# Kernel optimization log

Hardware: AMD Instinct MI355X
Metric: run time of the kernel (lower is better)

Reference implementation:

```python
import jax, jax.numpy as jnp
import numpy as np

B, T, F, U, L = 64, 700, 3, 400, 3


def setup_inputs() -> dict:
    key = jax.random.key(0)
    ks = jax.random.split(key, 10)
    s = 0.08  # small init to keep gates unsaturated
    return {
        "x": jax.random.normal(ks[0], (B, T, F), jnp.float32),
        "Wx0": jax.random.normal(ks[1], (F, 4 * U), jnp.float32) * s,
        "Wx1": jax.random.normal(ks[2], (U, 4 * U), jnp.float32) * s,
        "Wx2": jax.random.normal(ks[3], (U, 4 * U), jnp.float32) * s,
        "Wh": jax.random.normal(ks[4], (L, U, 4 * U), jnp.float32) * s,
        "b": jnp.zeros((L, 4 * U), jnp.float32),
        "pi": jax.random.normal(ks[5], (L, U), jnp.float32) * s,
        "pf": jax.random.normal(ks[6], (L, U), jnp.float32) * s,
        "po": jax.random.normal(ks[7], (L, U), jnp.float32) * s,
        "Wd": jax.random.normal(ks[8], (U, F), jnp.float32) * s,
        "bd": jnp.zeros((F,), jnp.float32),
    }


def _lstm_peephole_layer(x_tbd, Wx, Wh_l, b_l, pi_l, pf_l, po_l):
    """x_tbd: [T, B, D] -> [T, B, U] with peephole LSTM (Graves 2013)."""
    Bsz = x_tbd.shape[1]
    Uu = Wh_l.shape[0]
    # Precompute the input contribution for all timesteps in one GEMM.
    xp = jnp.einsum("tbd,dk->tbk", x_tbd, Wx) + b_l  # [T, B, 4U]

    def step(carry, zt):
        h, c = carry
        z = zt + h @ Wh_l  # [B, 4U]
        zi, zf, zg, zo = jnp.split(z, 4, axis=-1)
        i = jax.nn.sigmoid(zi + pi_l * c)
        f = jax.nn.sigmoid(zf + pf_l * c)
        c_new = f * c + i * jnp.tanh(zg)
        o = jax.nn.sigmoid(zo + po_l * c_new)
        h_new = o * jnp.tanh(c_new)
        return (h_new, c_new), h_new

    init = (jnp.zeros((Bsz, Uu), x_tbd.dtype), jnp.zeros((Bsz, Uu), x_tbd.dtype))
    _, hs = jax.lax.scan(step, init, xp)
    return hs  # [T, B, U]


def reference(x, Wx0, Wx1, Wx2, Wh, b, pi, pf, po, Wd, bd):
    h = jnp.transpose(x, (1, 0, 2))  # [T, B, F]
    for l, Wx in enumerate((Wx0, Wx1, Wx2)):
        h = _lstm_peephole_layer(h, Wx, Wh[l], b[l], pi[l], pf[l], po[l])
    out = jnp.einsum("tbu,uf->tbf", h, Wd) + bd
    return jnp.transpose(out, (1, 0, 2))  # [B, T, F]
```

## Files before the change

### kernel.cpp

```cpp
#include <hip/hip_runtime.h>
#include <hip/hip_fp16.h>
#include <math.h>

#define B_ 64
#define T_ 700
#define U_ 400
#define NF 704
#define FR_LS 13312

typedef _Float16 half8 __attribute__((ext_vector_type(8)));
typedef float float4v __attribute__((ext_vector_type(4)));

union AFrag { unsigned u[4]; half8 h; };

__device__ __forceinline__ unsigned agloadu(const unsigned* p) {
    return __hip_atomic_load(p, __ATOMIC_RELAXED, __HIP_MEMORY_SCOPE_AGENT);
}
__device__ __forceinline__ void agstoreu(unsigned* p, unsigned v) {
    __hip_atomic_store(p, v, __ATOMIC_RELAXED, __HIP_MEMORY_SCOPE_AGENT);
}
__device__ __forceinline__ float sig_(float v) {
    return __builtin_amdgcn_rcpf(1.f + __expf(-v));
}
__device__ __forceinline__ float tanh_(float v) {
    return 1.f - 2.f * __builtin_amdgcn_rcpf(__expf(2.f * v) + 1.f);
}
__device__ __forceinline__ void waitflag(const unsigned* f, unsigned target) {
    while (agloadu(f) < target) __builtin_amdgcn_s_sleep(2);
}
__device__ __forceinline__ unsigned f16u(float v) {
    union { _Float16 f; unsigned short s; } cv; cv.f = (_Float16)v; return (unsigned)cv.s;
}

__device__ __forceinline__ void pollfrag13(const unsigned* __restrict__ base,
                                           const unsigned par,
                                           AFrag* __restrict__ a, const int lane)
{
    {
        const unsigned* pp = base + (lane % 13) * 256 + ((lane * 37) & 255);
        while (!__all((int)(((agloadu(pp) ^ par) & 1u) == 0u)))
            __builtin_amdgcn_s_sleep(3);
    }
    unsigned pend = 0x1FFFu;
    do {
#pragma unroll
        for (int ck = 0; ck < 13; ++ck) if ((pend >> ck) & 1) {
#pragma unroll
            for (int d = 0; d < 4; ++d)
                a[ck].u[d] = agloadu(base + ck * 256 + d * 64 + lane);
        }
#pragma unroll
        for (int ck = 0; ck < 13; ++ck) if ((pend >> ck) & 1) {
            const unsigned m = (a[ck].u[0] ^ par) | (a[ck].u[1] ^ par)
                             | (a[ck].u[2] ^ par) | (a[ck].u[3] ^ par);
            if (__all((int)((m & 1u) == 0u))) pend &= ~(1u << ck);
        }
        if (pend) __builtin_amdgcn_s_sleep(3);
    } while (pend);
}

template<int DEPTH, int CP>
__global__ void __launch_bounds__(256, 1)
lstm_mix(const float* __restrict__ x,
         const float* __restrict__ Wx0,
         const float* __restrict__ Wx1,
         const float* __restrict__ Wx2,
         const float* __restrict__ Wh,
         const float* __restrict__ bias,
         const float* __restrict__ pi,
         const float* __restrict__ pf,
         const float* __restrict__ po,
         const float* __restrict__ Wd,
         const float* __restrict__ bd,
         float* __restrict__ out,
         unsigned* __restrict__ ws)
{
    __shared__ alignas(16) _Float16 wlds[26 * 512];
    __shared__ alignas(16) float zlds[4 * 528];
    __shared__ float gc[160];

    const int LW = NF * CP * 32;
    unsigned* F0 = ws;
    unsigned* F1 = F0 + LW;
    unsigned* F2 = F1 + LW;
    unsigned* FO = F2 + LW;
    unsigned* frag0 = ws + (size_t)4 * LW;

    const int blk  = blockIdx.x;
    const int tid  = threadIdx.x;
    const int lane = tid & 63;
    const int wv   = tid >> 6;
    const int cpi  = (blk + wv) & (CP - 1);

    int layer, u0;
    if      (blk < 50)  { layer = 0; u0 = blk * 8; }
    else if (blk < 150) { layer = 1; u0 = (blk - 50) * 4; }
    else if (blk < 250) { layer = 2; u0 = (blk - 150) * 4; }
    else                { layer = 3; u0 = 0; }

    const bool padw = (blk == 49) || (blk == 149) || (blk == 249);
    int pad_off[2];
    {
        const int i0 = tid, i1 = tid + 256;
        pad_off[0] = (i0 >> 7) * 3328 + 12 * 256 + (((i0 >> 4) & 3) * 64)
                   + (2 + ((i0 >> 6) & 1)) * 16 + (i0 & 15);
        pad_off[1] = (i1 >> 7) * 3328 + 12 * 256 + (((i1 >> 4) & 3) * 64)
                   + (2 + ((i1 >> 6) & 1)) * 16 + (i1 & 15);
    }

    {
        const float* __restrict__ Wxl = (layer == 1) ? Wx1 : Wx2;
        for (int i = tid; i < 26 * 64; i += 256) {
            const int ln = i & 63, ck = i >> 6;
            const int q = ln >> 4, nn = ln & 15;
            float vals[8];
#pragma unroll
            for (int j = 0; j < 8; ++j) {
                const int kc = ck % 13;
                const int k = kc * 32 + q * 8 + j;
                float v = 0.f;
                if (k < 400) {
                    if (layer == 0) {
                        const int col32 = (ck / 13) * 16 + nn;
                        const int gcol = (col32 >> 3) * U_ + u0 + (col32 & 7);
                        v = Wh[(size_t)k * 1600 + gcol];
                    } else if (layer < 3) {
                        const int gcol = (nn >> 2) * U_ + u0 + (nn & 3);
                        v = (ck >= 13) ? Wh[((size_t)layer * U_ + k) * 1600 + gcol]
                                       : Wxl[(size_t)k * 1600 + gcol];
                    } else {
                        if (ck < 13 && nn < 3) v = Wd[k * 3 + nn];
                    }
                }
                vals[j] = v;
            }
#pragma unroll
            for (int j = 0; j < 8; ++j)
                wlds[ck * 512 + ln * 8 + j] = (_Float16)vals[j];
        }
        if (layer == 0) {
            if (tid < 128) {
                const int col32 = tid >> 2, comp = tid & 3;
                const int gcol = (col32 >> 3) * U_ + u0 + (col32 & 7);
                gc[tid] = (comp == 0) ? bias[gcol] : Wx0[(size_t)(comp - 1) * 1600 + gcol];
            } else if (tid < 152) {
                const int idx = tid - 128, ul = idx / 3, j = idx - ul * 3;
                const float* pp = (j == 0) ? pi : (j == 1) ? pf : po;
                gc[tid] = pp[u0 + ul];
            }
        } else if (layer < 3) {
            if (tid < 16) {
                gc[tid] = bias[layer * 1600 + (tid >> 2) * U_ + u0 + (tid & 3)];
            } else if (tid < 28) {
                const int idx = tid - 16, ul = idx / 3, j = idx - ul * 3;
                const float* pp = (j == 0) ? pi : (j == 1) ? pf : po;
                gc[tid] = pp[layer * U_ + u0 + ul];
            }
        } else {
            if (tid < 3) gc[tid] = bd[tid];
        }
    }
    __syncthreads();

    const int wvz   = wv * 528;
    const int b_loc = lane & 15;
    const int quad  = lane >> 4;
    float cst[2] = {0.f, 0.f};

    for (int t = 0; t < T_; ++t) {
        const int sw = t % DEPTH;
        const int sr = (t + DEPTH - 1) % DEPTH;
        const unsigned pI = (unsigned)((t / DEPTH) & 1);
        const unsigned pO = (unsigned)(((t - 1) / DEPTH) & 1);

        float x0, x1, x2;
        if (layer == 0) {
            const size_t xb = (size_t)(wv * 16 + b_loc) * T_ + t;
            x0 = x[xb * 3 + 0]; x1 = x[xb * 3 + 1]; x2 = x[xb * 3 + 2];
        }

        if (lane == 0) {
            if (layer == 0) {
                if (wv == 0 && t >= DEPTH) waitflag(F1 + ((t - DEPTH) * CP + cpi) * 32, 100);
            } else if (layer == 1) {
                waitflag(F0 + (t * CP + cpi) * 32, 50);
                if (wv == 0 && t >= DEPTH) waitflag(F2 + ((t - DEPTH) * CP + cpi) * 32, 100);
            } else if (layer == 2) {
                waitflag(F1 + (t * CP + cpi) * 32, 100);
                if (wv == 0 && t >= DEPTH) waitflag(FO + ((t - DEPTH) * CP + cpi) * 32, 1);
            } else {
                waitflag(F2 + (t * CP + cpi) * 32, 100);
            }
        }
        asm volatile("" ::: "memory");

        AFrag ainp[13];
        if (layer == 1 || layer == 2) {
            const unsigned* frI = frag0 + (size_t)((layer - 1) * DEPTH + sw) * FR_LS + wv * 3328;
#pragma unroll
            for (int kc = 0; kc < 13; ++kc)
#pragma unroll
                for (int d = 0; d < 4; ++d)
                    ainp[kc].u[d] = agloadu(frI + kc * 256 + d * 64 + lane);
        }

        AFrag aown[13];
        if (layer == 3) {
            const unsigned* frI = frag0 + (size_t)(2 * DEPTH + sw) * FR_LS + wv * 3328;
#pragma unroll
            for (int kc = 0; kc < 13; ++kc)
#pragma unroll
                for (int d = 0; d < 4; ++d)
                    aown[kc].u[d] = agloadu(frI + kc * 256 + d * 64 + lane);
        } else if (t >= 1) {
            const unsigned* frO = frag0 + (size_t)(layer * DEPTH + sr) * FR_LS + wv * 3328;
            pollfrag13(frO, pO, aown, lane);
        } else {
#pragma unroll
            for (int kc = 0; kc < 13; ++kc)
#pragma unroll
                for (int d = 0; d < 4; ++d) aown[kc].u[d] = 0u;
        }
        asm volatile("" ::: "memory");

        if (layer == 0) {
            float4v acc0 = {0.f, 0.f, 0.f, 0.f}, acc1 = {0.f, 0.f, 0.f, 0.f};
#pragma unroll
            for (int kc = 0; kc < 13; ++kc) {
                const half8 w0 = *(const half8*)&wlds[kc * 512 + lane * 8];
                const half8 w1 = *(const half8*)&wlds[(13 + kc) * 512 + lane * 8];
                acc0 = __builtin_amdgcn_mfma_f32_16x16x32_f16(aown[kc].h, w0, acc0, 0, 0, 0);
                acc1 = __builtin_amdgcn_mfma_f32_16x16x32_f16(aown[kc].h, w1, acc1, 0, 0, 0);
            }
#pragma unroll
            for (int r = 0; r < 4; ++r) {
                zlds[wvz + (quad * 4 + r) * 33 + b_loc] = acc0[r];
                zlds[wvz + (quad * 4 + r) * 33 + 16 + b_loc] = acc1[r];
            }
        } else if (layer < 3) {
            float4v acc = {0.f, 0.f, 0.f, 0.f};
#pragma unroll
            for (int kc = 0; kc < 13; ++kc) {
                const half8 wA = *(const half8*)&wlds[kc * 512 + lane * 8];
                const half8 wB = *(const half8*)&wlds[(13 + kc) * 512 + lane * 8];
                acc = __builtin_amdgcn_mfma_f32_16x16x32_f16(ainp[kc].h, wA, acc, 0, 0, 0);
                acc = __builtin_amdgcn_mfma_f32_16x16x32_f16(aown[kc].h, wB, acc, 0, 0, 0);
            }
#pragma unroll
            for (int r = 0; r < 4; ++r)
                zlds[wvz + (quad * 4 + r) * 33 + b_loc] = acc[r];
        } else {
            float4v acc = {0.f, 0.f, 0.f, 0.f};
#pragma unroll
            for (int kc = 0; kc < 13; ++kc) {
                const half8 w0 = *(const half8*)&wlds[kc * 512 + lane * 8];
                acc = __builtin_amdgcn_mfma_f32_16x16x32_f16(aown[kc].h, w0, acc, 0, 0, 0);
            }
            if (b_loc < 3) {
#pragma unroll
                for (int r = 0; r < 4; ++r)
                    out[((size_t)(wv * 16 + quad * 4 + r) * T_ + t) * 3 + b_loc] = acc[r] + gc[b_loc];
            }
        }
        __syncthreads();

        if (padw) {
            unsigned* fr_dst = frag0 + (size_t)(layer * DEPTH + sw) * FR_LS;
            agstoreu(fr_dst + pad_off[0], pI);
            agstoreu(fr_dst + pad_off[1], pI);
        }

        if (layer == 0) {
            unsigned* fr_dst = frag0 + (size_t)(0 * DEPTH + sw) * FR_LS + wv * 3328;
#pragma unroll
            for (int q = 0; q < 2; ++q) {
                const int ul = q * 4 + quad;
                const int ug = u0 + ul;
                float z[4];
#pragma unroll
                for (int g = 0; g < 4; ++g) {
                    const int gb = (g * 8 + ul) * 4;
                    z[g] = zlds[wvz + b_loc * 33 + g * 8 + ul]
                         + gc[gb + 0] + x0 * gc[gb + 1] + x1 * gc[gb + 2] + x2 * gc[gb + 3];
                }
                const float cp = cst[q];
                const float ig = sig_(z[0] + gc[128 + ul * 3 + 0] * cp);
                const float fg = sig_(z[1] + gc[128 + ul * 3 + 1] * cp);
                const float cn = fg * cp + ig * tanh_(z[2]);
                const float og = sig_(z[3] + gc[128 + ul * 3 + 2] * cn);
                cst[q] = cn;
                const float hv = og * tanh_(cn);
                const float pv = __shfl_xor(hv, 16, 64);
                if ((quad & 1) == 0) {
                    const unsigned pw_ = ((f16u(hv) & ~1u) | pI) | (f16u(pv) << 16);
                    const int u = ug;
                    agstoreu(fr_dst + (u >> 5) * 256 + ((u & 7) >> 1) * 64
                                    + ((u >> 3) & 3) * 16 + b_loc, pw_);
                }
            }
        } else if (layer < 3) {
            unsigned* fr_dst = frag0 + (size_t)(layer * DEPTH + sw) * FR_LS + wv * 3328;
            const int ul = quad;
            float z[4];
#pragma unroll
            for (int g = 0; g < 4; ++g)
                z[g] = zlds[wvz + b_loc * 33 + g * 4 + ul] + gc[g * 4 + ul];
            const float cp = cst[0];
            const float ig = sig_(z[0] + gc[16 + ul * 3 + 0] * cp);
            const float fg = sig_(z[1] + gc[16 + ul * 3 + 1] * cp);
            const float cn = fg * cp + ig * tanh_(z[2]);
            const float og = sig_(z[3] + gc[16 + ul * 3 + 2] * cn);
            cst[0] = cn;
            const float hv = og * tanh_(cn);
            const float pv = __shfl_xor(hv, 16, 64);
            if ((ul & 1) == 0) {
                const unsigned pw_ = ((f16u(hv) & ~1u) | pI) | (f16u(pv) << 16);
                const int u = u0 + ul;
                agstoreu(fr_dst + (u >> 5) * 256 + ((u & 7) >> 1) * 64
                                + ((u >> 3) & 3) * 16 + b_loc, pw_);
            }
        }

        asm volatile("s_waitcnt vmcnt(0)" ::: "memory");
        __syncthreads();
        if (tid < CP) {
            unsigned* f = (layer == 0) ? F0 : (layer == 1) ? F1
                        : (layer == 2) ? F2 : FO;
            __hip_atomic_fetch_add(f + (t * CP + tid) * 32, 1u,
                                   __ATOMIC_RELAXED, __HIP_MEMORY_SCOPE_AGENT);
        }
    }
}

template<int DEPTH, int CP>
static void launch_variant(void* const* d_in, float* out, unsigned* ws, hipStream_t stream) {
    const float* x    = (const float*)d_in[0];
    const float* Wx0  = (const float*)d_in[1];
    const float* Wx1  = (const float*)d_in[2];
    const float* Wx2  = (const float*)d_in[3];
    const float* Wh   = (const float*)d_in[4];
    const float* bias = (const float*)d_in[5];
    const float* pi   = (const float*)d_in[6];
    const float* pf   = (const float*)d_in[7];
    const float* po   = (const float*)d_in[8];
    const float* Wd   = (const float*)d_in[9];
    const float* bd   = (const float*)d_in[10];
    void* args[] = { (void*)&x, (void*)&Wx0, (void*)&Wx1, (void*)&Wx2, (void*)&Wh,
                     (void*)&bias, (void*)&pi, (void*)&pf, (void*)&po,
                     (void*)&Wd, (void*)&bd, (void*)&out, (void*)&ws };
    hipError_t err = hipLaunchCooperativeKernel((void*)lstm_mix<DEPTH, CP>,
                                                dim3(251), dim3(256), args, 0, stream);
    if (err != hipSuccess)
        hipLaunchKernelGGL((lstm_mix<DEPTH, CP>), dim3(251), dim3(256), 0, stream,
                           x, Wx0, Wx1, Wx2, Wh, bias, pi, pf, po, Wd, bd, out, ws);
}

extern "C" void kernel_launch(void* const* d_in, const int* in_sizes, int n_in,
                              void* d_out, int out_size, void* d_ws, size_t ws_size,
                              hipStream_t stream) {
    float* out = (float*)d_out;
    unsigned* ws = (unsigned*)d_ws;

    auto flagbytes = [](int cp) -> size_t { return (size_t)4 * NF * cp * 32 * 4; };
    auto fragbytes = [](int depth) -> size_t { return (size_t)3 * depth * FR_LS * 4; };

    if (ws_size >= flagbytes(8) + fragbytes(8)) {
        hipMemsetAsync(d_ws, 0, flagbytes(8), stream);
        hipMemsetAsync((char*)d_ws + flagbytes(8), 0xFF, fragbytes(8), stream);
        launch_variant<8, 8>(d_in, out, ws, stream);
    } else if (ws_size >= flagbytes(4) + fragbytes(4)) {
        hipMemsetAsync(d_ws, 0, flagbytes(4), stream);
        hipMemsetAsync((char*)d_ws + flagbytes(4), 0xFF, fragbytes(4), stream);
        launch_variant<4, 4>(d_in, out, ws, stream);
    } else {
        hipMemsetAsync(d_ws, 0, flagbytes(2), stream);
        hipMemsetAsync((char*)d_ws + flagbytes(2), 0xFF, fragbytes(2), stream);
        launch_variant<2, 2>(d_in, out, ws, stream);
    }
}
```

Before: 2.852 ms.

## Replace atomic counter flags with per-producer flag slots polled by wave vote

Each producer block now writes its own flag word with a plain relaxed store instead of atomically incrementing a shared counter. Consumers poll all producer slots with a whole wavefront and use __all to check that every slot is nonzero. This is meant to remove atomic contention on hot counters. Replica count drops from 8 to 2, so each flag array is 128 words wide. The trade-off is more polling loads per wait and a larger flag workspace to memset.

```diff
diff --git a/kernel.cpp b/kernel.cpp
--- a/kernel.cpp
+++ b/kernel.cpp
@@ -25,11 +25,22 @@
 __device__ __forceinline__ float tanh_(float v) {
     return 1.f - 2.f * __builtin_amdgcn_rcpf(__expf(2.f * v) + 1.f);
 }
-__device__ __forceinline__ void waitflag(const unsigned* f, unsigned target) {
-    while (agloadu(f) < target) __builtin_amdgcn_s_sleep(2);
-}
 __device__ __forceinline__ unsigned f16u(float v) {
     union { _Float16 f; unsigned short s; } cv; cv.f = (_Float16)v; return (unsigned)cv.s;
+}
+
+__device__ __forceinline__ void votenz(const unsigned* f, const int lane, const int n) {
+    for (;;) {
+        bool ok = true;
+        const unsigned a = agloadu(f + lane);
+        if (lane < n) ok = (a != 0u);
+        if (n > 64) {
+            const unsigned b = agloadu(f + 64 + lane);
+            if (64 + lane < n) ok = ok && (b != 0u);
+        }
+        if (__all((int)ok)) break;
+        __builtin_amdgcn_s_sleep(2);
+    }
 }
 
 __device__ __forceinline__ void pollfrag13(const unsigned* __restrict__ base,
@@ -79,7 +90,7 @@
     __shared__ alignas(16) float zlds[4 * 528];
     __shared__ float gc[160];
 
-    const int LW = NF * CP * 32;
+    const int LW = NF * CP * 128;
     unsigned* F0 = ws;
     unsigned* F1 = F0 + LW;
     unsigned* F2 = F1 + LW;
@@ -90,13 +101,13 @@
     const int tid  = threadIdx.x;
     const int lane = tid & 63;
     const int wv   = tid >> 6;
-    const int cpi  = (blk + wv) & (CP - 1);
-
-    int layer, u0;
-    if      (blk < 50)  { layer = 0; u0 = blk * 8; }
-    else if (blk < 150) { layer = 1; u0 = (blk - 50) * 4; }
-    else if (blk < 250) { layer = 2; u0 = (blk - 150) * 4; }
-    else                { layer = 3; u0 = 0; }
+    const int rep  = (blk + wv) & (CP - 1);
+
+    int layer, u0, rk;
+    if      (blk < 50)  { layer = 0; rk = blk;       u0 = blk * 8; }
+    else if (blk < 150) { layer = 1; rk = blk - 50;  u0 = (blk - 50) * 4; }
+    else if (blk < 250) { layer = 2; rk = blk - 150; u0 = (blk - 150) * 4; }
+    else                { layer = 3; rk = 0;         u0 = 0; }
 
     const bool padw = (blk == 49) || (blk == 149) || (blk == 249);
     int pad_off[2];
@@ -179,18 +190,19 @@
             x0 = x[xb * 3 + 0]; x1 = x[xb * 3 + 1]; x2 = x[xb * 3 + 2];
         }
 
-        if (lane == 0) {
-            if (layer == 0) {
-                if (wv == 0 && t >= DEPTH) waitflag(F1 + ((t - DEPTH) * CP + cpi) * 32, 100);
-            } else if (layer == 1) {
-                waitflag(F0 + (t * CP + cpi) * 32, 50);
-                if (wv == 0 && t >= DEPTH) waitflag(F2 + ((t - DEPTH) * CP + cpi) * 32, 100);
-            } else if (layer == 2) {
-                waitflag(F1 + (t * CP + cpi) * 32, 100);
-                if (wv == 0 && t >= DEPTH) waitflag(FO + ((t - DEPTH) * CP + cpi) * 32, 1);
-            } else {
-                waitflag(F2 + (t * CP + cpi) * 32, 100);
-            }
+        if (layer == 0) {
+            if (wv == 0 && t >= DEPTH)
+                votenz(F1 + ((size_t)(t - DEPTH) * CP + rep) * 128, lane, 100);
+        } else if (layer == 1) {
+            votenz(F0 + ((size_t)t * CP + rep) * 128, lane, 50);
+            if (wv == 0 && t >= DEPTH)
+                votenz(F2 + ((size_t)(t - DEPTH) * CP + rep) * 128, lane, 100);
+        } else if (layer == 2) {
+            votenz(F1 + ((size_t)t * CP + rep) * 128, lane, 100);
+            if (wv == 0 && t >= DEPTH)
+                votenz(FO + ((size_t)(t - DEPTH) * CP + rep) * 128, lane, 1);
+        } else {
+            votenz(F2 + ((size_t)t * CP + rep) * 128, lane, 100);
         }
         asm volatile("" ::: "memory");
 
@@ -326,8 +338,7 @@
         if (tid < CP) {
             unsigned* f = (layer == 0) ? F0 : (layer == 1) ? F1
                         : (layer == 2) ? F2 : FO;
-            __hip_atomic_fetch_add(f + (t * CP + tid) * 32, 1u,
-                                   __ATOMIC_RELAXED, __HIP_MEMORY_SCOPE_AGENT);
+            agstoreu(f + ((size_t)t * CP + tid) * 128 + rk, 1u);
         }
     }
 }
@@ -361,20 +372,20 @@
     float* out = (float*)d_out;
     unsigned* ws = (unsigned*)d_ws;
 
-    auto flagbytes = [](int cp) -> size_t { return (size_t)4 * NF * cp * 32 * 4; };
+    auto flagbytes = [](int cp) -> size_t { return (size_t)4 * NF * cp * 128 * 4; };
     auto fragbytes = [](int depth) -> size_t { return (size_t)3 * depth * FR_LS * 4; };
 
-    if (ws_size >= flagbytes(8) + fragbytes(8)) {
-        hipMemsetAsync(d_ws, 0, flagbytes(8), stream);
-        hipMemsetAsync((char*)d_ws + flagbytes(8), 0xFF, fragbytes(8), stream);
-        launch_variant<8, 8>(d_in, out, ws, stream);
-    } else if (ws_size >= flagbytes(4) + fragbytes(4)) {
-        hipMemsetAsync(d_ws, 0, flagbytes(4), stream);
-        hipMemsetAsync((char*)d_ws + flagbytes(4), 0xFF, fragbytes(4), stream);
-        launch_variant<4, 4>(d_in, out, ws, stream);
+    if (ws_size >= flagbytes(2) + fragbytes(8)) {
+        hipMemsetAsync(d_ws, 0, flagbytes(2), stream);
+        hipMemsetAsync((char*)d_ws + flagbytes(2), 0xFF, fragbytes(8), stream);
+        launch_variant<8, 2>(d_in, out, ws, stream);
+    } else if (ws_size >= flagbytes(1) + fragbytes(4)) {
+        hipMemsetAsync(d_ws, 0, flagbytes(1), stream);
+        hipMemsetAsync((char*)d_ws + flagbytes(1), 0xFF, fragbytes(4), stream);
+        launch_variant<4, 1>(d_in, out, ws, stream);
     } else {
-        hipMemsetAsync(d_ws, 0, flagbytes(2), stream);
-        hipMemsetAsync((char*)d_ws + flagbytes(2), 0xFF, fragbytes(2), stream);
-        launch_variant<2, 2>(d_in, out, ws, stream);
-    }
-}
+        hipMemsetAsync(d_ws, 0, flagbytes(1), stream);
+        hipMemsetAsync((char*)d_ws + flagbytes(1), 0xFF, fragbytes(2), stream);
+        launch_variant<2, 1>(d_in, out, ws, stream);
+    }
+}
```

Measured after the change: 2.790 ms. 2.2% less time.
